# Performance work log

Measured on AMD Instinct MI355X. Metric: run time of the kernel, lower is better.

## Reference

```python
import jax, jax.numpy as jnp
import numpy as np

N, E, F_IN, D, B = 20000, 50000, 16, 64, 128


def setup_inputs() -> dict:
    key = jax.random.key(0)
    ks = jax.random.split(key, 24)
    s = 0.05
    inp = {
        "x": jax.random.normal(ks[0], (N, F_IN), jnp.float32),
        "edge_index": jax.random.randint(ks[1], (2, E), 0, N, jnp.int32),
        "edge_attr": jax.random.uniform(ks[2], (E, 5), jnp.float32),
        "batch": jnp.sort(jax.random.randint(ks[3], (N,), 0, B, jnp.int32)),
        # lin0
        "lin0_w": jax.random.normal(ks[4], (D, F_IN)) * s,
        "lin0_b": jnp.zeros((D,), jnp.float32),
        # edge MLP: Linear(5,128) -> ReLU -> Linear(128, D*D)
        "mlp_w1": jax.random.normal(ks[5], (128, 5)) * s,
        "mlp_b1": jnp.zeros((128,), jnp.float32),
        "mlp_w2": jax.random.normal(ks[6], (D * D, 128)) * s,
        "mlp_b2": jnp.zeros((D * D,), jnp.float32),
        # NNConv bias (root_weight=False, bias=True)
        "conv_b": jnp.zeros((D,), jnp.float32),
        # GRU(dim, dim), single layer
        "gru_w_ih": jax.random.normal(ks[7], (3 * D, D)) * s,
        "gru_w_hh": jax.random.normal(ks[8], (3 * D, D)) * s,
        "gru_b_ih": jnp.zeros((3 * D,), jnp.float32),
        "gru_b_hh": jnp.zeros((3 * D,), jnp.float32),
        # Set2Set LSTM(2*dim, dim)
        "lstm_w_ih": jax.random.normal(ks[9], (4 * D, 2 * D)) * s,
        "lstm_w_hh": jax.random.normal(ks[10], (4 * D, D)) * s,
        "lstm_b_ih": jnp.zeros((4 * D,), jnp.float32),
        "lstm_b_hh": jnp.zeros((4 * D,), jnp.float32),
    }
    return inp


def _gru_cell(x, h, w_ih, w_hh, b_ih, b_hh):
    gi = x @ w_ih.T + b_ih
    gh = h @ w_hh.T + b_hh
    i_r, i_z, i_n = jnp.split(gi, 3, axis=-1)
    h_r, h_z, h_n = jnp.split(gh, 3, axis=-1)
    r = jax.nn.sigmoid(i_r + h_r)
    z = jax.nn.sigmoid(i_z + h_z)
    n = jnp.tanh(i_n + r * h_n)
    return (1.0 - z) * n + z * h


def _lstm_cell(x, h, c, w_ih, w_hh, b_ih, b_hh):
    g = x @ w_ih.T + b_ih + h @ w_hh.T + b_hh
    i, f, gg, o = jnp.split(g, 4, axis=-1)
    c_new = jax.nn.sigmoid(f) * c + jax.nn.sigmoid(i) * jnp.tanh(gg)
    h_new = jax.nn.sigmoid(o) * jnp.tanh(c_new)
    return h_new, c_new


def reference(x, edge_index, edge_attr, batch,
              lin0_w, lin0_b, mlp_w1, mlp_b1, mlp_w2, mlp_b2, conv_b,
              gru_w_ih, gru_w_hh, gru_b_ih, gru_b_hh,
              lstm_w_ih, lstm_w_hh, lstm_b_ih, lstm_b_hh):
    src, dst = edge_index[0], edge_index[1]

    out = jax.nn.relu(x @ lin0_w.T + lin0_b)  # [N, D]
    h = out  # GRU hidden (seq_len=1 -> out == h after each step)

    # Edge-conditioned weights: MLP(edge_attr) -> [E, D, D]
    hidden = jax.nn.relu(edge_attr @ mlp_w1.T + mlp_b1)
    W_e = (hidden @ mlp_w2.T + mlp_b2).reshape(E, D, D)

    # in-degree counts for mean aggregation
    deg = jax.ops.segment_sum(jnp.ones((E,), x.dtype), dst, num_segments=N)
    deg = jnp.maximum(deg, 1.0)[:, None]

    for _ in range(3):
        # NNConv: gather src feats, per-edge matmul, scatter-mean to dst
        msg = jnp.einsum('ed,edo->eo', out[src], W_e)  # [E, D]
        agg = jax.ops.segment_sum(msg, dst, num_segments=N) / deg
        m = jax.nn.relu(agg + conv_b)
        h = _gru_cell(m, h, gru_w_ih, gru_w_hh, gru_b_ih, gru_b_hh)
        out = h

    # Set2Set pooling, 3 processing steps
    q_star = jnp.zeros((B, 2 * D), x.dtype)
    hh = jnp.zeros((B, D), x.dtype)
    cc = jnp.zeros((B, D), x.dtype)
    for _ in range(3):
        hh, cc = _lstm_cell(q_star, hh, cc, lstm_w_ih, lstm_w_hh, lstm_b_ih, lstm_b_hh)
        q = hh  # [B, D]
        e = jnp.sum(out * q[batch], axis=-1)  # [N]
        e_max = jax.ops.segment_max(e, batch, num_segments=B)
        a = jnp.exp(e - e_max[batch])
        a = a / jax.ops.segment_sum(a, batch, num_segments=B)[batch]
        r = jax.ops.segment_sum(a[:, None] * out, batch, num_segments=B)  # [B, D]
        q_star = jnp.concatenate([q, r], axis=-1)

    return q_star  # [B, 2*D]
```

## Files before the change

kernel.cpp:

```cpp
#include <hip/hip_runtime.h>
#include <hip/hip_bf16.h>

typedef float BF;
__device__ __forceinline__ float ldf(const BF* p, int i) { return p[i]; }

typedef _Float16 h8 __attribute__((ext_vector_type(8)));
typedef float f4 __attribute__((ext_vector_type(4)));

static constexpr int N_NODES = 20000;
static constexpr int N_EDGES = 50000;
static constexpr int E_PAD   = 50176;
static constexpr int N_MSGB  = 196;
static constexpr int N_PAD   = 20032;
static constexpr int BROW    = 136;
static constexpr int SROW    = 72;
static constexpr int N_B     = 79;
static constexpr int MAXSEG  = 2048;

__device__ __forceinline__ float sigf(float x) { return 1.f / (1.f + __expf(-x)); }
__device__ __forceinline__ float tanh_f(float x) {
  float e = __expf(2.f * x);
  return 1.f - 2.f / (e + 1.f);
}

static constexpr int S1_LIN0 = 5000;
static constexpr int S1_QS   = 2048;
static constexpr int S1_WCAT = 128;
static constexpr int S1_B2S  = 16;
static constexpr int S1_DEG  = 196;
static constexpr int PREP1_BLOCKS = S1_LIN0 + S1_QS + S1_WCAT + S1_B2S + 1 + 1 + S1_DEG;

__global__ void k_prep1(const BF* __restrict__ x, const int* __restrict__ batch,
                        const int* __restrict__ dst,
                        const BF* __restrict__ w0, const BF* __restrict__ b0,
                        const BF* __restrict__ w2, const BF* __restrict__ b2,
                        const BF* __restrict__ gwih, const BF* __restrict__ gwhh,
                        const BF* __restrict__ gbih, const BF* __restrict__ gbhh,
                        float* __restrict__ h, _Float16* __restrict__ h16,
                        _Float16* __restrict__ Qs, _Float16* __restrict__ Wcat,
                        float* __restrict__ bcat, _Float16* __restrict__ b2s,
                        int* __restrict__ seg, int* __restrict__ degi,
                        int* __restrict__ bsum) {
  int bid = blockIdx.x, t = threadIdx.x;
  if (bid < S1_LIN0) {
    __shared__ float xs[64];
    if (t < 64) xs[t] = ldf(x, bid * 64 + t);
    __syncthreads();
    int nl = t >> 6, o = t & 63;
    float acc = ldf(b0, o);
#pragma unroll
    for (int f = 0; f < 16; ++f) acc += xs[nl * 16 + f] * ldf(w0, o * 16 + f);
    float v = fmaxf(acc, 0.f);
    int idx = bid * 256 + t;
    h[idx] = v;
    h16[idx] = (_Float16)v;
    return;
  }
  bid -= S1_LIN0;
  if (bid < S1_QS) {
    int i = bid * 256 + t;
    int j = i & 7, ln = (i >> 3) & 63, f8 = (i >> 9) & 7;
    int dl = (i >> 12) & 63, oh = i >> 18;
    int tk = f8 >> 1, ctl = f8 & 1;
    int o = oh * 32 + ctl * 16 + (ln & 15);
    int k = tk * 32 + (ln >> 4) * 8 + j;
    Qs[i] = (_Float16)ldf(w2, (dl * 64 + o) * 128 + k);
    return;
  }
  bid -= S1_QS;
  if (bid < S1_WCAT) {
    int idx = bid * 256 + t, row = idx >> 7, k = idx & 127;
    int g = row >> 6, rr = row & 63;
    float v = 0.f;
    if (g == 0) v = (k < 64) ? ldf(gwih, rr * 64 + k) : ldf(gwhh, rr * 64 + (k - 64));
    else if (g == 1) v = (k < 64) ? ldf(gwih, (64 + rr) * 64 + k) : ldf(gwhh, (64 + rr) * 64 + (k - 64));
    else if (g == 2) v = (k < 64) ? ldf(gwih, (128 + rr) * 64 + k) : 0.f;
    else v = (k < 64) ? 0.f : ldf(gwhh, (128 + rr) * 64 + (k - 64));
    Wcat[idx] = (_Float16)v;
    return;
  }
  bid -= S1_WCAT;
  if (bid < S1_B2S) {
    int idx = bid * 256 + t;
    int f = idx >> 9, ln = (idx >> 3) & 63, j = idx & 7;
    int o = (f & 3) * 16 + (ln & 15);
    int d = (f >> 2) * 32 + (ln >> 4) * 8 + j;
    b2s[idx] = (_Float16)ldf(b2, d * 64 + o);
    return;
  }
  bid -= S1_B2S;
  if (bid == 0) {
    float v;
    if (t < 128) v = ldf(gbih, t) + ldf(gbhh, t);
    else if (t < 192) v = ldf(gbih, t);
    else v = ldf(gbhh, t - 64);
    bcat[t] = v;
    return;
  }
  bid -= 1;
  if (bid == 0) {
    if (t > 128) return;
    if (t == 128) { seg[128] = N_NODES; return; }
    int lo = 0, hi = N_NODES;
    while (lo < hi) {
      int mid = (lo + hi) >> 1;
      if (batch[mid] < t) lo = mid + 1; else hi = mid;
    }
    seg[t] = lo;
    return;
  }
  bid -= 1;
  {
    int e = bid * 256 + t;
    if (e < N_EDGES) {
      int d = dst[e];
      atomicAdd(&degi[d], 1);
      atomicAdd(&bsum[d >> 8], 1);
    }
  }
}

__global__ void k_scanA(const int* __restrict__ bsum, int* __restrict__ boff) {
  __shared__ int sd[128];
  int t = threadIdx.x;
  int x = (t < N_B) ? bsum[t] : 0;
  sd[t] = x;
  __syncthreads();
#pragma unroll
  for (int o = 1; o < 128; o <<= 1) {
    int val = (t >= o) ? sd[t - o] : 0;
    __syncthreads();
    sd[t] += val;
    __syncthreads();
  }
  if (t < N_B) boff[t] = sd[t] - x;
}

__global__ void k_scanB(const int* __restrict__ degi, const int* __restrict__ boff,
                        int* __restrict__ cursor) {
  __shared__ int sd[256];
  int b = blockIdx.x, t = threadIdx.x;
  int v = b * 256 + t;
  int x = (v < N_NODES) ? degi[v] : 0;
  sd[t] = x;
  __syncthreads();
#pragma unroll
  for (int o = 1; o < 256; o <<= 1) {
    int val = (t >= o) ? sd[t - o] : 0;
    __syncthreads();
    sd[t] += val;
    __syncthreads();
  }
  if (v < N_NODES) cursor[v] = boff[b] + sd[t] - x;
}

__global__ void k_fill(const int* __restrict__ dst, int* __restrict__ cursor,
                       int* __restrict__ eperm) {
  int e = blockIdx.x * 256 + threadIdx.x;
  if (e < N_EDGES) {
    int pos = atomicAdd(&cursor[dst[e]], 1);
    eperm[pos] = e;
  }
}

static constexpr int S2_MLP = E_PAD / 8;
static constexpr int S2_SP  = 196;

__global__ void k_prep2(const BF* __restrict__ ea, const int* __restrict__ src,
                        const int* __restrict__ dst, const int* __restrict__ eperm,
                        const BF* __restrict__ w1, const BF* __restrict__ b1,
                        _Float16* __restrict__ hidf, int* __restrict__ spadp,
                        int* __restrict__ dpadp) {
  int bid = blockIdx.x, t = threadIdx.x;
  if (bid < S2_MLP) {
    __shared__ float eas[40];
    __shared__ int el8[8];
    if (t < 8) { int pos = bid * 8 + t; el8[t] = (pos < N_EDGES) ? eperm[pos] : -1; }
    __syncthreads();
    if (t < 40) { int e = el8[t / 5]; eas[t] = (e >= 0) ? ldf(ea, e * 5 + (t % 5)) : 0.f; }
    __syncthreads();
#pragma unroll
    for (int rep = 0; rep < 4; ++rep) {
      int item = t + rep * 256;
      int le = item >> 7, j = item & 127;
      int pos = bid * 8 + le;
      float v = 0.f;
      if (pos < N_EDGES) {
        float acc = ldf(b1, j);
#pragma unroll
        for (int i = 0; i < 5; ++i) acc += eas[le * 5 + i] * ldf(w1, j * 5 + i);
        v = fmaxf(acc, 0.f);
      }
      hidf[(size_t)pos * 128 + j] = (_Float16)v;
    }
    return;
  }
  bid -= S2_MLP;
  {
    int pos = bid * 256 + t;
    if (pos < E_PAD) {
      int e = (pos < N_EDGES) ? eperm[pos] : -1;
      spadp[pos] = (e >= 0) ? src[e] : 0;
      dpadp[pos] = (e >= 0) ? dst[e] : 0;
    }
  }
}

__launch_bounds__(256, 2)
__global__ void k_msg(const _Float16* __restrict__ h16, const _Float16* __restrict__ hidf,
                      const _Float16* __restrict__ Qs, const _Float16* __restrict__ b2s,
                      const int* __restrict__ spadp, const int* __restrict__ dpadp,
                      float* __restrict__ agg) {
  __shared__ _Float16 s_lds[256 * SROW];
  __shared__ _Float16 b_lds[2][4096];
  __shared__ _Float16 b2l[2048];
  const int tid = threadIdx.x;
  const int wv = tid >> 6, ln = tid & 63;
  const int m0 = ln & 15, quad = ln >> 4;
  const int tb = blockIdx.x * 256;
  const int oh = blockIdx.y;

  {
    int sp_ = spadp[tb + tid];
    const uint4* hp4 = (const uint4*)(h16 + (size_t)sp_ * 64);
#pragma unroll
    for (int c = 0; c < 8; ++c) *(uint4*)&s_lds[tid * SROW + c * 8] = hp4[c];
  }
  {
    int frag = tid >> 6, wi = tid & 63;
    int tp = frag >> 1, ctl = frag & 1;
    int sf = (tp << 2) | (oh * 2 + ctl);
    *(uint4*)&b2l[frag * 512 + wi * 8] = *((const uint4*)b2s + sf * 64 + wi);
  }
  h8 hvv[4][4];
#pragma unroll
  for (int mt = 0; mt < 4; ++mt) {
    int e = tb + wv * 64 + mt * 16 + m0;
    const _Float16* hp = hidf + (size_t)e * 128 + quad * 8;
#pragma unroll
    for (int c = 0; c < 4; ++c) hvv[mt][c] = *(const h8*)(hp + c * 32);
  }
  uint4 breg[2];
  {
    const uint4* qb = (const uint4*)(Qs + (size_t)(oh * 64) * 4096);
    breg[0] = qb[tid];
    breg[1] = qb[tid + 256];
    *(uint4*)&b_lds[0][tid * 8] = breg[0];
    *(uint4*)&b_lds[0][(tid + 256) * 8] = breg[1];
  }
  __syncthreads();

  f4 acc[4][2];
#pragma unroll
  for (int mt = 0; mt < 4; ++mt)
#pragma unroll
    for (int ct = 0; ct < 2; ++ct)
#pragma unroll
      for (int j = 0; j < 4; ++j) acc[mt][ct][j] = 0.f;

  for (int dl = 0; dl < 64; ++dl) {
    int cur = dl & 1;
    if (dl < 63) {
      const uint4* qb = (const uint4*)(Qs + (size_t)(oh * 64 + dl + 1) * 4096);
      breg[0] = qb[tid];
      breg[1] = qb[tid + 256];
    }
    _Float16 sv[4];
#pragma unroll
    for (int mt = 0; mt < 4; ++mt)
      sv[mt] = s_lds[(wv * 64 + mt * 16 + m0) * SROW + dl];
#pragma unroll
    for (int tk = 0; tk < 4; ++tk) {
      h8 a[4];
#pragma unroll
      for (int mt = 0; mt < 4; ++mt) a[mt] = hvv[mt][tk] * sv[mt];
#pragma unroll
      for (int ctl = 0; ctl < 2; ++ctl) {
        h8 b = *(const h8*)&b_lds[cur][(tk * 2 + ctl) * 512 + ln * 8];
#pragma unroll
        for (int mt = 0; mt < 4; ++mt)
          acc[mt][ctl] = __builtin_amdgcn_mfma_f32_16x16x32_f16(a[mt], b, acc[mt][ctl], 0, 0, 0);
      }
    }
    if (dl < 63) {
      *(uint4*)&b_lds[cur ^ 1][tid * 8] = breg[0];
      *(uint4*)&b_lds[cur ^ 1][(tid + 256) * 8] = breg[1];
    }
    __syncthreads();
  }
#pragma unroll
  for (int tp = 0; tp < 2; ++tp) {
    h8 a[4];
#pragma unroll
    for (int mt = 0; mt < 4; ++mt)
      a[mt] = *(const h8*)&s_lds[(wv * 64 + mt * 16 + m0) * SROW + tp * 32 + quad * 8];
#pragma unroll
    for (int ctl = 0; ctl < 2; ++ctl) {
      h8 b = *(const h8*)&b2l[(tp * 2 + ctl) * 512 + ln * 8];
#pragma unroll
      for (int mt = 0; mt < 4; ++mt)
        acc[mt][ctl] = __builtin_amdgcn_mfma_f32_16x16x32_f16(a[mt], b, acc[mt][ctl], 0, 0, 0);
    }
  }
#pragma unroll
  for (int mt = 0; mt < 4; ++mt) {
#pragma unroll
    for (int r = 0; r < 4; ++r) {
      int pos = tb + wv * 64 + mt * 16 + quad * 4 + r;
      if (pos < N_EDGES) {
        float* ap = agg + (size_t)dpadp[pos] * 64 + oh * 32 + m0;
        atomicAdd(ap, acc[mt][0][r]);
        atomicAdd(ap + 16, acc[mt][1][r]);
      }
    }
  }
}

__launch_bounds__(256)
__global__ void k_gru(float* __restrict__ agg, const int* __restrict__ degi,
                      const BF* __restrict__ convb, const _Float16* __restrict__ W,
                      const float* __restrict__ bcat, float* __restrict__ h,
                      _Float16* __restrict__ h16) {
  __shared__ _Float16 xa[64 * BROW];
  __shared__ _Float16 wb[256 * BROW];
  __shared__ float bsh[256];
  int tid = threadIdx.x;
  int wv = tid >> 6, ln = tid & 63, m0 = ln & 15, quad = ln >> 4;
  int rowblk = blockIdx.x * 64;
  bsh[tid] = bcat[tid];
  {
    int r = tid >> 2, c0 = (tid & 3) * 16;
    int node = rowblk + r;
    _Float16 mv[16], hv[16];
    if (node < N_NODES) {
      float inv = 1.f / (float)max(degi[node], 1);
      float* ap = agg + (size_t)node * 64 + c0;
      const float* hp = h + (size_t)node * 64 + c0;
#pragma unroll
      for (int i = 0; i < 16; i += 4) {
        float4 a = *(float4*)(ap + i);
        *(float4*)(ap + i) = make_float4(0.f, 0.f, 0.f, 0.f);
        float4 hf = *(const float4*)(hp + i);
        mv[i + 0] = (_Float16)fmaxf(a.x * inv + ldf(convb, c0 + i + 0), 0.f);
        mv[i + 1] = (_Float16)fmaxf(a.y * inv + ldf(convb, c0 + i + 1), 0.f);
        mv[i + 2] = (_Float16)fmaxf(a.z * inv + ldf(convb, c0 + i + 2), 0.f);
        mv[i + 3] = (_Float16)fmaxf(a.w * inv + ldf(convb, c0 + i + 3), 0.f);
        hv[i + 0] = (_Float16)hf.x; hv[i + 1] = (_Float16)hf.y;
        hv[i + 2] = (_Float16)hf.z; hv[i + 3] = (_Float16)hf.w;
      }
    } else {
#pragma unroll
      for (int i = 0; i < 16; ++i) { mv[i] = (_Float16)0.f; hv[i] = (_Float16)0.f; }
    }
    *(uint4*)&xa[r * BROW + c0] = *(const uint4*)&mv[0];
    *(uint4*)&xa[r * BROW + c0 + 8] = *(const uint4*)&mv[8];
    *(uint4*)&xa[r * BROW + 64 + c0] = *(const uint4*)&hv[0];
    *(uint4*)&xa[r * BROW + 64 + c0 + 8] = *(const uint4*)&hv[8];
  }
#pragma unroll
  for (int c = 0; c < 16; ++c) {
    int i = tid + c * 256, r = i >> 4, ch = i & 15;
    *(uint4*)&wb[r * BROW + ch * 8] = *(const uint4*)(W + (size_t)r * 128 + ch * 8);
  }
  __syncthreads();
  f4 acc[16];
#pragma unroll
  for (int ct = 0; ct < 16; ++ct)
#pragma unroll
    for (int j = 0; j < 4; ++j) acc[ct][j] = 0.f;
#pragma unroll
  for (int t = 0; t < 4; ++t) {
    h8 a = *(const h8*)&xa[(wv * 16 + m0) * BROW + t * 32 + quad * 8];
#pragma unroll
    for (int ct = 0; ct < 16; ++ct) {
      h8 b = *(const h8*)&wb[(ct * 16 + m0) * BROW + t * 32 + quad * 8];
      acc[ct] = __builtin_amdgcn_mfma_f32_16x16x32_f16(a, b, acc[ct], 0, 0, 0);
    }
  }
#pragma unroll
  for (int c0 = 0; c0 < 4; ++c0) {
    int o = c0 * 16 + m0;
    float br = bsh[o], bz = bsh[64 + o], bn = bsh[128 + o], bh2 = bsh[192 + o];
#pragma unroll
    for (int r = 0; r < 4; ++r) {
      int row = rowblk + wv * 16 + quad * 4 + r;
      if (row < N_NODES) {
        float rr = sigf(acc[c0][r] + br);
        float zz = sigf(acc[c0 + 4][r] + bz);
        float nn = tanh_f(acc[c0 + 8][r] + bn + rr * (acc[c0 + 12][r] + bh2));
        size_t hi = (size_t)row * 64 + o;
        float hp = h[hi];
        float hn = (1.f - zz) * nn + zz * hp;
        h[hi] = hn;
        h16[hi] = (_Float16)hn;
      }
    }
  }
}

__launch_bounds__(1024)
__global__ void k_s2s(const float* __restrict__ h, const int* __restrict__ seg,
                      const BF* __restrict__ wih, const BF* __restrict__ whh,
                      const BF* __restrict__ bih, const BF* __restrict__ bhh,
                      float* __restrict__ outp) {
  __shared__ float xrow[128], g[256], qrow[64], hc[64], ccs[64], rr_[64];
  __shared__ float evals[MAXSEG];
  __shared__ float wred[16], wred2[16], rpart[16 * 64];
  int b = blockIdx.x, t = threadIdx.x;
  int wv = t >> 6, ln = t & 63;
  if (t < 64) { hc[t] = 0.f; ccs[t] = 0.f; rr_[t] = 0.f; }
  __syncthreads();
  int start = seg[b], end = seg[b + 1];
  int cnt = end - start;
  for (int st = 0; st < 3; ++st) {
    if (t < 64) xrow[t] = hc[t];
    else if (t < 128) xrow[t] = rr_[t - 64];
    __syncthreads();
    if (t < 256) {
      float acc = ldf(bih, t) + ldf(bhh, t);
      const float4* wr4 = (const float4*)(wih + t * 128);
#pragma unroll
      for (int i = 0; i < 32; ++i) {
        float4 wv4 = wr4[i];
        acc += xrow[i * 4] * wv4.x + xrow[i * 4 + 1] * wv4.y +
               xrow[i * 4 + 2] * wv4.z + xrow[i * 4 + 3] * wv4.w;
      }
      const float4* wr2 = (const float4*)(whh + t * 64);
#pragma unroll
      for (int i = 0; i < 16; ++i) {
        float4 wv4 = wr2[i];
        acc += xrow[i * 4] * wv4.x + xrow[i * 4 + 1] * wv4.y +
               xrow[i * 4 + 2] * wv4.z + xrow[i * 4 + 3] * wv4.w;
      }
      g[t] = acc;
    }
    __syncthreads();
    if (t < 64) {
      float ig = sigf(g[t]), fg = sigf(g[64 + t]);
      float gg = tanh_f(g[128 + t]), og = sigf(g[192 + t]);
      float c = fg * ccs[t] + ig * gg;
      ccs[t] = c;
      float hn = og * tanh_f(c);
      hc[t] = hn;
      qrow[t] = hn;
    }
    __syncthreads();
    float q = qrow[ln];
    float mw = -3.4e38f;
    for (int n0 = start + wv * 2; n0 < end; n0 += 32) {
      int n1 = n0 + 1;
      float p0 = h[(size_t)n0 * 64 + ln] * q;
      float p1 = (n1 < end) ? h[(size_t)n1 * 64 + ln] * q : 0.f;
#pragma unroll
      for (int off = 32; off > 0; off >>= 1) {
        p0 += __shfl_xor(p0, off);
        p1 += __shfl_xor(p1, off);
      }
      if (ln == 0) {
        evals[n0 - start] = p0;
        mw = fmaxf(mw, p0);
        if (n1 < end) { evals[n1 - start] = p1; mw = fmaxf(mw, p1); }
      }
    }
    if (ln == 0) wred[wv] = mw;
    __syncthreads();
    float gmax = -3.4e38f;
#pragma unroll
    for (int i = 0; i < 16; ++i) gmax = fmaxf(gmax, wred[i]);
    __syncthreads();
    float psum = 0.f;
    for (int i = t; i < cnt; i += 1024) {
      float a = __expf(evals[i] - gmax);
      evals[i] = a;
      psum += a;
    }
#pragma unroll
    for (int off = 32; off > 0; off >>= 1) psum += __shfl_xor(psum, off);
    if (ln == 0) wred2[wv] = psum;
    __syncthreads();
    float tsum = 0.f;
#pragma unroll
    for (int i = 0; i < 16; ++i) tsum += wred2[i];
    float inv = 1.f / fmaxf(tsum, 1e-30f);
    float racc = 0.f;
    for (int n0 = start + wv * 2; n0 < end; n0 += 32) {
      int n1 = n0 + 1;
      float a0 = evals[n0 - start] * h[(size_t)n0 * 64 + ln];
      float a1 = (n1 < end) ? evals[n1 - start] * h[(size_t)n1 * 64 + ln] : 0.f;
      racc += a0 + a1;
    }
    rpart[wv * 64 + ln] = racc;
    __syncthreads();
    if (t < 64) {
      float s = 0.f;
#pragma unroll
      for (int i = 0; i < 16; ++i) s += rpart[i * 64 + t];
      rr_[t] = s * inv;
    }
    __syncthreads();
  }
  if (t < 128) outp[b * 128 + t] = (t < 64) ? hc[t] : rr_[t - 64];
}

extern "C" void kernel_launch(void* const* d_in, const int* in_sizes, int n_in,
                              void* d_out, int out_size, void* d_ws, size_t ws_size,
                              hipStream_t stream) {
  const BF* x      = (const BF*)d_in[0];
  const int* ei    = (const int*)d_in[1];
  const BF* ea     = (const BF*)d_in[2];
  const int* batch = (const int*)d_in[3];
  const BF* w0     = (const BF*)d_in[4];
  const BF* b0     = (const BF*)d_in[5];
  const BF* w1     = (const BF*)d_in[6];
  const BF* b1     = (const BF*)d_in[7];
  const BF* w2     = (const BF*)d_in[8];
  const BF* b2     = (const BF*)d_in[9];
  const BF* convb  = (const BF*)d_in[10];
  const BF* gwih   = (const BF*)d_in[11];
  const BF* gwhh   = (const BF*)d_in[12];
  const BF* gbih   = (const BF*)d_in[13];
  const BF* gbhh   = (const BF*)d_in[14];
  const BF* lwih   = (const BF*)d_in[15];
  const BF* lwhh   = (const BF*)d_in[16];
  const BF* lbih   = (const BF*)d_in[17];
  const BF* lbhh   = (const BF*)d_in[18];
  const int* src = ei;
  const int* dstp = ei + N_EDGES;

  char* w = (char*)d_ws;
  size_t off_b = 0;
  auto take = [&](size_t bytes) -> void* {
    void* p = w + off_b;
    off_b = (off_b + bytes + 255) & ~(size_t)255;
    return p;
  };
  _Float16* Qs   = (_Float16*)take((size_t)4096 * 128 * 2);
  _Float16* hidf = (_Float16*)take((size_t)E_PAD * 128 * 2);
  float* h       = (float*)take((size_t)N_NODES * 64 * 4);
  _Float16* h16  = (_Float16*)take((size_t)N_NODES * 64 * 2);
  float* zr      = (float*)take((size_t)(N_NODES * 64 + N_NODES + 128) * 4);
  float* agg     = zr;
  int*   degi    = (int*)(zr + N_NODES * 64);
  int*   bsum    = degi + N_NODES;
  _Float16* Wcat = (_Float16*)take((size_t)256 * 128 * 2);
  float* bcat    = (float*)take((size_t)256 * 4);
  _Float16* b2s  = (_Float16*)take((size_t)8 * 512 * 2);
  int*   seg     = (int*)take((size_t)129 * 4);
  int*   boff    = (int*)take((size_t)128 * 4);
  int*   cursor  = (int*)take((size_t)N_NODES * 4);
  int*   eperm   = (int*)take((size_t)N_EDGES * 4);
  int*   spadp   = (int*)take((size_t)E_PAD * 4);
  int*   dpadp   = (int*)take((size_t)E_PAD * 4);

  hipMemsetAsync(zr, 0, (size_t)(N_NODES * 64 + N_NODES + 128) * 4, stream);
  k_prep1<<<PREP1_BLOCKS, 256, 0, stream>>>(x, batch, dstp, w0, b0, w2, b2,
                                            gwih, gwhh, gbih, gbhh,
                                            h, h16, Qs, Wcat, bcat, b2s,
                                            seg, degi, bsum);
  k_scanA<<<1, 128, 0, stream>>>(bsum, boff);
  k_scanB<<<N_B, 256, 0, stream>>>(degi, boff, cursor);
  k_fill<<<196, 256, 0, stream>>>(dstp, cursor, eperm);
  k_prep2<<<S2_MLP + S2_SP, 256, 0, stream>>>(ea, src, dstp, eperm, w1, b1,
                                              hidf, spadp, dpadp);
  for (int it = 0; it < 3; ++it) {
    k_msg<<<dim3(N_MSGB, 2), 256, 0, stream>>>(h16, hidf, Qs, b2s, spadp, dpadp, agg);
    k_gru<<<N_PAD / 64, 256, 0, stream>>>(agg, degi, convb, Wcat, bcat, h, h16);
  }
  k_s2s<<<128, 1024, 0, stream>>>(h, seg, lwih, lwhh, lbih, lbhh, (float*)d_out);
}
```

Before: 443.5 us.

## Load edge-MLP weight fragments directly from global into registers, drop LDS double buffer

The message kernel used to stage each dl slice of the Qs weight tensor through a double-buffered LDS array, with a block-wide barrier on every one of the 64 iterations. Now each wave reads its MFMA B fragments straight from global (cached) memory into registers, and the per-row scale factors are fetched eight at a time as a vector from LDS. This removes 64 barriers and the LDS traffic, and frees LDS for occupancy. In exchange all four waves load the same weights redundantly from L1/L2, and more global-load latency is exposed without explicit prefetching.

After: 534.8 us. 1.21x slower.

```diff
diff --git a/kernel.cpp b/kernel.cpp
--- a/kernel.cpp
+++ b/kernel.cpp
@@ -212,7 +212,6 @@
                       const int* __restrict__ spadp, const int* __restrict__ dpadp,
                       float* __restrict__ agg) {
   __shared__ _Float16 s_lds[256 * SROW];
-  __shared__ _Float16 b_lds[2][4096];
   __shared__ _Float16 b2l[2048];
   const int tid = threadIdx.x;
   const int wv = tid >> 6, ln = tid & 63;
@@ -240,14 +239,6 @@
 #pragma unroll
     for (int c = 0; c < 4; ++c) hvv[mt][c] = *(const h8*)(hp + c * 32);
   }
-  uint4 breg[2];
-  {
-    const uint4* qb = (const uint4*)(Qs + (size_t)(oh * 64) * 4096);
-    breg[0] = qb[tid];
-    breg[1] = qb[tid + 256];
-    *(uint4*)&b_lds[0][tid * 8] = breg[0];
-    *(uint4*)&b_lds[0][(tid + 256) * 8] = breg[1];
-  }
   __syncthreads();
 
   f4 acc[4][2];
@@ -258,35 +249,32 @@
 #pragma unroll
       for (int j = 0; j < 4; ++j) acc[mt][ct][j] = 0.f;
 
-  for (int dl = 0; dl < 64; ++dl) {
-    int cur = dl & 1;
-    if (dl < 63) {
-      const uint4* qb = (const uint4*)(Qs + (size_t)(oh * 64 + dl + 1) * 4096);
-      breg[0] = qb[tid];
-      breg[1] = qb[tid + 256];
-    }
-    _Float16 sv[4];
+  const _Float16* qbase = Qs + (size_t)(oh * 64) * 4096 + (size_t)ln * 8;
+  for (int dlb = 0; dlb < 8; ++dlb) {
+    h8 sv8[4];
 #pragma unroll
     for (int mt = 0; mt < 4; ++mt)
-      sv[mt] = s_lds[(wv * 64 + mt * 16 + m0) * SROW + dl];
-#pragma unroll
-    for (int tk = 0; tk < 4; ++tk) {
-      h8 a[4];
-#pragma unroll
-      for (int mt = 0; mt < 4; ++mt) a[mt] = hvv[mt][tk] * sv[mt];
-#pragma unroll
-      for (int ctl = 0; ctl < 2; ++ctl) {
-        h8 b = *(const h8*)&b_lds[cur][(tk * 2 + ctl) * 512 + ln * 8];
-#pragma unroll
-        for (int mt = 0; mt < 4; ++mt)
-          acc[mt][ctl] = __builtin_amdgcn_mfma_f32_16x16x32_f16(a[mt], b, acc[mt][ctl], 0, 0, 0);
-      }
-    }
-    if (dl < 63) {
-      *(uint4*)&b_lds[cur ^ 1][tid * 8] = breg[0];
-      *(uint4*)&b_lds[cur ^ 1][(tid + 256) * 8] = breg[1];
-    }
-    __syncthreads();
+      sv8[mt] = *(const h8*)&s_lds[(wv * 64 + mt * 16 + m0) * SROW + dlb * 8];
+#pragma unroll
+    for (int dli = 0; dli < 8; ++dli) {
+      const _Float16* qd = qbase + (size_t)(dlb * 8 + dli) * 4096;
+      h8 bf[8];
+#pragma unroll
+      for (int f = 0; f < 8; ++f) bf[f] = *(const h8*)(qd + f * 512);
+#pragma unroll
+      for (int tk = 0; tk < 4; ++tk) {
+        h8 a[4];
+#pragma unroll
+        for (int mt = 0; mt < 4; ++mt) a[mt] = hvv[mt][tk] * sv8[mt][dli];
+#pragma unroll
+        for (int ctl = 0; ctl < 2; ++ctl) {
+          h8 b = bf[tk * 2 + ctl];
+#pragma unroll
+          for (int mt = 0; mt < 4; ++mt)
+            acc[mt][ctl] = __builtin_amdgcn_mfma_f32_16x16x32_f16(a[mt], b, acc[mt][ctl], 0, 0, 0);
+        }
+      }
+    }
   }
 #pragma unroll
   for (int tp = 0; tp < 2; ++tp) {
```
